# Optimization experiments

Measured on AMD Instinct MI355X. Metric: run time of the kernel, lower is better.

Reference implementation:

```python
import jax, jax.numpy as jnp
import numpy as np

B, S, E, H = 4, 2048, 1024, 16
D = E // H  # head dim = 64


def setup_inputs() -> dict:
    key = jax.random.key(0)
    ks = jax.random.split(key, 5)
    scale = 0.02
    return {
        "x": jax.random.normal(ks[0], (B, S, E), dtype=jnp.float32),
        "Wa_w": jax.random.normal(ks[1], (3 * E, E), dtype=jnp.float32) * scale,
        "Wa_b": jax.random.normal(ks[2], (3 * E,), dtype=jnp.float32) * scale,
        "Wo_w": jax.random.normal(ks[3], (E, E), dtype=jnp.float32) * scale,
        "Wo_b": jax.random.normal(ks[4], (E,), dtype=jnp.float32) * scale,
    }


def reference(x, Wa_w, Wa_b, Wo_w, Wo_b):
    b, s, e = x.shape
    # Fused QKV projection (torch Linear: x @ W^T + b)
    qkv = jnp.einsum("bse,fe->bsf", x, Wa_w) + Wa_b  # [B,S,3E]
    q, k, v = jnp.split(qkv, 3, axis=-1)
    # [B,S,E] -> [B,H,S,D]
    def heads(t):
        return t.reshape(b, s, H, D).transpose(0, 2, 1, 3)
    q, k, v = heads(q), heads(k), heads(v)
    # Causal attention with explicit score matrix (as in the original)
    scores = jnp.einsum("bhqd,bhkd->bhqk", q, k) / jnp.sqrt(jnp.float32(D))
    causal = jnp.tril(jnp.ones((s, s), dtype=bool))
    scores = jnp.where(causal, scores, -jnp.inf)
    attn = jax.nn.softmax(scores, axis=-1)  # dropout p=0 -> identity
    out = jnp.einsum("bhqk,bhkd->bhqd", attn, v)  # [B,H,S,D]
    out = out.transpose(0, 2, 1, 3).reshape(b, s, e)
    return jnp.einsum("bse,fe->bsf", out, Wo_w) + Wo_b
```

## Files before the change

### kernel.cpp

```cpp
#include <hip/hip_runtime.h>
#include <hip/hip_bf16.h>
#include <cstdint>

typedef __bf16 bf16_t;
typedef __attribute__((ext_vector_type(8))) __bf16 bf16x8;
typedef __attribute__((ext_vector_type(4))) __bf16 bf16x4;
typedef __attribute__((ext_vector_type(4))) float f32x4;

#define B_ 4
#define S_ 2048
#define E_ 1024
#define H_ 16
#define D_ 64

#define QSCALE 0.18033688011112042f

__global__ void cvt_f32_to_bf16(const float* __restrict__ in, bf16_t* __restrict__ out, int n4) {
    int i = blockIdx.x * blockDim.x + threadIdx.x;
    int stride = gridDim.x * blockDim.x;
    for (; i < n4; i += stride) {
        f32x4 v = reinterpret_cast<const f32x4*>(in)[i];
        bf16x4 o;
        o.x = (bf16_t)v.x; o.y = (bf16_t)v.y; o.z = (bf16_t)v.z; o.w = (bf16_t)v.w;
        reinterpret_cast<bf16x4*>(out)[i] = o;
    }
}

__device__ __forceinline__ void gload_lds16(const bf16_t* g, bf16_t* l) {
    __builtin_amdgcn_global_load_lds((const __attribute__((address_space(1))) void*)g,
                                     (__attribute__((address_space(3))) void*)l, 16, 0, 0);
}

template <int MODE>
__launch_bounds__(256)
__global__ void gemm_bt(const bf16_t* __restrict__ A, const bf16_t* __restrict__ Bm,
                        const float* __restrict__ bias,
                        int M, int N, int K,
                        bf16_t* __restrict__ Qg, bf16_t* __restrict__ Kg,
                        bf16_t* __restrict__ Vtg, float* __restrict__ Outf) {
    const int BM = 128, BN = 128, BK = 32;
    __shared__ __align__(16) bf16_t As[2][BM * BK];
    __shared__ __align__(16) bf16_t Bs[2][BN * BK];

    const int nwg = gridDim.x;
    const int cpx = nwg >> 3;
    const int bid = (blockIdx.x & 7) * cpx + (blockIdx.x >> 3);

    const int nTilesN = N / BN;
    const int mt = bid / nTilesN, nt = bid % nTilesN;
    const int m0 = mt * BM, n0 = nt * BN;
    const int t = threadIdx.x;
    const int lane = t & 63;
    const int wid = t >> 6;
    const int wr = wid >> 1, wc = wid & 1;
    const int lr = lane & 15, lg = lane >> 4;

    const int row = t >> 2;
    const int chunk = t & 3;
    const bf16_t* aSrc0 = A + (int64_t)(m0 + row) * K + chunk * 8;
    const bf16_t* bSrc0 = Bm + (int64_t)(n0 + row) * K + chunk * 8;
    const int ldsOff = row * BK + chunk * 8;

    auto stage = [&](int buf, int kt) {
        const bf16_t* a = aSrc0 + kt * BK;
        const bf16_t* b = bSrc0 + kt * BK;
        gload_lds16(a, &As[buf][ldsOff]);
        gload_lds16(a + (int64_t)64 * K, &As[buf][ldsOff + 64 * BK]);
        gload_lds16(b, &Bs[buf][ldsOff]);
        gload_lds16(b + (int64_t)64 * K, &Bs[buf][ldsOff + 64 * BK]);
    };

    f32x4 acc[4][4] = {};

    stage(0, 0);
    __syncthreads();
    const int nk = K / BK;
    for (int kt = 0; kt < nk; ++kt) {
        int buf = kt & 1;
        if (kt + 1 < nk) stage(buf ^ 1, kt + 1);
        bf16x8 af[4], bfr[4];
        const int ko = lg * 8;
#pragma unroll
        for (int i = 0; i < 4; ++i) {
            af[i]  = *(const bf16x8*)&As[buf][(wr * 64 + i * 16 + lr) * BK + ko];
            bfr[i] = *(const bf16x8*)&Bs[buf][(wc * 64 + i * 16 + lr) * BK + ko];
        }
#pragma unroll
        for (int i = 0; i < 4; ++i)
#pragma unroll
            for (int j = 0; j < 4; ++j)
                acc[i][j] = __builtin_amdgcn_mfma_f32_16x16x32_bf16(af[i], bfr[j], acc[i][j], 0, 0, 0);
        __syncthreads();
    }

    if (MODE == 0) {
        const int which = n0 / E_;
#pragma unroll
        for (int j = 0; j < 4; ++j) {
            const int f = n0 + wc * 64 + j * 16 + lr;
            const float bv = bias[f];
            const int fe = f - which * E_;
            const int h = fe >> 6, d = fe & 63;
#pragma unroll
            for (int i = 0; i < 4; ++i) {
#pragma unroll
                for (int r = 0; r < 4; ++r) {
                    const int m = m0 + wr * 64 + i * 16 + lg * 4 + r;
                    const int b = m >> 11, si = m & (S_ - 1);
                    const float v = acc[i][j][r] + bv;
                    if (which == 0)
                        Qg[(((int64_t)(b * H_ + h)) * S_ + si) * D_ + d] = (bf16_t)(v * QSCALE);
                    else if (which == 1)
                        Kg[(((int64_t)(b * H_ + h)) * S_ + si) * D_ + d] = (bf16_t)v;
                    else
                        Vtg[(((int64_t)(b * H_ + h)) * D_ + d) * S_ + si] = (bf16_t)v;
                }
            }
        }
    } else {
#pragma unroll
        for (int j = 0; j < 4; ++j) {
            const int f = n0 + wc * 64 + j * 16 + lr;
            const float bv = bias[f];
#pragma unroll
            for (int i = 0; i < 4; ++i) {
#pragma unroll
                for (int r = 0; r < 4; ++r) {
                    const int m = m0 + wr * 64 + i * 16 + lg * 4 + r;
                    Outf[(int64_t)m * N + f] = acc[i][j][r] + bv;
                }
            }
        }
    }
}

__launch_bounds__(256, 4)
__global__ void attn_causal(const bf16_t* __restrict__ Qg, const bf16_t* __restrict__ Kg,
                            const bf16_t* __restrict__ Vtg, bf16_t* __restrict__ Og) {
    __shared__ __align__(16) bf16_t Ks[2][64 * 64];
    __shared__ __align__(16) bf16_t Vs[2][64 * 64];
    __shared__ __align__(16) bf16_t P_lds[4][16 * 64];

    const int bid = blockIdx.x;
    const int xcd = bid & 7, j = bid >> 3;
    const int bh = (j >> 4) * 8 + xcd;
    const int i = j & 15;
    const int qtA = i, qtB = 31 - i;

    const int t = threadIdx.x, lane = t & 63, w = t >> 6;
    const int lr = lane & 15, lg = lane >> 4;
    const int q0A = qtA * 64 + w * 16;
    const int q0B = qtB * 64 + w * 16;

    const bf16_t* Qb = Qg + (int64_t)bh * S_ * D_;
    const bf16_t* Kb = Kg + (int64_t)bh * S_ * D_;
    const bf16_t* Vb = Vtg + (int64_t)bh * D_ * S_;

    const int srow = t >> 3;
    const int scol_sw = (t & 7) ^ (srow & 7);

    auto stageK = [&](int buf, int kv0) {
        const bf16_t* base = Kb + (kv0 + srow) * D_ + scol_sw * 8;
        gload_lds16(base, &Ks[buf][t * 8]);
        gload_lds16(base + 32 * D_, &Ks[buf][t * 8 + 2048]);
    };
    auto stageV = [&](int buf, int kv0) {
        const bf16_t* base = Vb + srow * S_ + kv0 + scol_sw * 8;
        gload_lds16(base, &Vs[buf][t * 8]);
        gload_lds16(base + 32 * S_, &Vs[buf][t * 8 + 2048]);
    };

    auto psw = [](int row, int col) {
        return row * 64 + ((((col >> 3) ^ (row & 7)) << 3) | (col & 7));
    };

    bf16x8 qfA[2], qfB[2];
#pragma unroll
    for (int kk = 0; kk < 2; ++kk) {
        qfA[kk] = *(const bf16x8*)&Qb[(q0A + lr) * D_ + kk * 32 + lg * 8];
        qfB[kk] = *(const bf16x8*)&Qb[(q0B + lr) * D_ + kk * 32 + lg * 8];
    }

    bf16x8 ones;
#pragma unroll
    for (int e = 0; e < 8; ++e) ones[e] = (bf16_t)1.0f;

    f32x4 oA[4] = {}, oB[4] = {};
    f32x4 lA = {}, lB = {};

    int cur = 0;
    stageK(0, 0);
    stageV(0, 0);
    __syncthreads();

    for (int tkv = 0; tkv <= qtB; ++tkv) {
        const int kv0 = tkv * 64;
        if (tkv < qtB) { stageK(cur ^ 1, kv0 + 64); stageV(cur ^ 1, kv0 + 64); }

        auto process = [&](int q0, const bf16x8* qf, f32x4* o, f32x4& accl, bf16_t* Pw) {
            f32x4 sc[4] = {};
            __builtin_amdgcn_s_setprio(1);
#pragma unroll
            for (int nj = 0; nj < 4; ++nj) {
                if (kv0 + nj * 16 <= q0 + 15) {
                    const int krow = nj * 16 + lr;
#pragma unroll
                    for (int kk = 0; kk < 2; ++kk) {
                        bf16x8 kfr = *(const bf16x8*)&Ks[cur][krow * 64 + (((kk * 4 + lg) ^ (krow & 7)) * 8)];
                        sc[nj] = __builtin_amdgcn_mfma_f32_16x16x32_bf16(qf[kk], kfr, sc[nj], 0, 0, 0);
                    }
                }
            }
            __builtin_amdgcn_s_setprio(0);

            if (kv0 + 64 > q0) {
#pragma unroll
                for (int nj = 0; nj < 4; ++nj) {
                    const int col = kv0 + nj * 16 + lr;
#pragma unroll
                    for (int r = 0; r < 4; ++r) {
                        const int rowg = q0 + lg * 4 + r;
                        if (col > rowg) sc[nj][r] = -1e30f;
                    }
                }
            }

#pragma unroll
            for (int nj = 0; nj < 4; ++nj)
#pragma unroll
                for (int r = 0; r < 4; ++r)
                    Pw[psw(lg * 4 + r, nj * 16 + lr)] = (bf16_t)__builtin_amdgcn_exp2f(sc[nj][r]);
            asm volatile("s_waitcnt lgkmcnt(0)" ::: "memory");
            __builtin_amdgcn_sched_barrier(0);

            __builtin_amdgcn_s_setprio(1);
#pragma unroll
            for (int kk = 0; kk < 2; ++kk) {
                bf16x8 pa = *(const bf16x8*)&Pw[psw(lr, kk * 32 + lg * 8)];
                accl = __builtin_amdgcn_mfma_f32_16x16x32_bf16(pa, ones, accl, 0, 0, 0);
#pragma unroll
                for (int nd = 0; nd < 4; ++nd) {
                    const int vrow = nd * 16 + lr;
                    bf16x8 vf = *(const bf16x8*)&Vs[cur][vrow * 64 + (((kk * 4 + lg) ^ (vrow & 7)) * 8)];
                    o[nd] = __builtin_amdgcn_mfma_f32_16x16x32_bf16(pa, vf, o[nd], 0, 0, 0);
                }
            }
            __builtin_amdgcn_s_setprio(0);
        };

        process(q0B, qfB, oB, lB, &P_lds[w][0]);
        if (tkv <= qtA) process(q0A, qfA, oA, lA, &P_lds[w][0]);

        __syncthreads();
        cur ^= 1;
    }

    const int b = bh >> 4, h = bh & 15;
#pragma unroll
    for (int r = 0; r < 4; ++r) {
        const float rlA = 1.0f / lA[r];
        const float rlB = 1.0f / lB[r];
        const int rA = q0A + lg * 4 + r;
        const int rB = q0B + lg * 4 + r;
#pragma unroll
        for (int nd = 0; nd < 4; ++nd) {
            Og[((int64_t)(b * S_ + rA)) * E_ + h * D_ + nd * 16 + lr] = (bf16_t)(oA[nd][r] * rlA);
            Og[((int64_t)(b * S_ + rB)) * E_ + h * D_ + nd * 16 + lr] = (bf16_t)(oB[nd][r] * rlB);
        }
    }
}

extern "C" void kernel_launch(void* const* d_in, const int* in_sizes, int n_in,
                              void* d_out, int out_size, void* d_ws, size_t ws_size,
                              hipStream_t stream) {
    const float* x    = (const float*)d_in[0];
    const float* Wa_w = (const float*)d_in[1];
    const float* Wa_b = (const float*)d_in[2];
    const float* Wo_w = (const float*)d_in[3];
    const float* Wo_b = (const float*)d_in[4];
    float* out = (float*)d_out;

    const size_t M = (size_t)B_ * S_;
    char* ws = (char*)d_ws;
    bf16_t* xb  = (bf16_t*)ws; ws += M * E_ * 2;
    bf16_t* wab = (bf16_t*)ws; ws += (size_t)3 * E_ * E_ * 2;
    bf16_t* wob = (bf16_t*)ws; ws += (size_t)E_ * E_ * 2;
    bf16_t* Qg  = (bf16_t*)ws; ws += M * E_ * 2;
    bf16_t* Kg  = (bf16_t*)ws; ws += M * E_ * 2;
    bf16_t* Vtg = (bf16_t*)ws; ws += M * E_ * 2;
    bf16_t* Og  = (bf16_t*)ws; ws += M * E_ * 2;

    cvt_f32_to_bf16<<<2048, 256, 0, stream>>>(x, xb, (int)(M * E_ / 4));
    cvt_f32_to_bf16<<<768, 256, 0, stream>>>(Wa_w, wab, 3 * E_ * E_ / 4);
    cvt_f32_to_bf16<<<256, 256, 0, stream>>>(Wo_w, wob, E_ * E_ / 4);

    gemm_bt<0><<<(8192 / 128) * (3072 / 128), 256, 0, stream>>>(
        xb, wab, Wa_b, 8192, 3072, 1024, Qg, Kg, Vtg, nullptr);

    attn_causal<<<B_ * H_ * 16, 256, 0, stream>>>(Qg, Kg, Vtg, Og);

    gemm_bt<1><<<(8192 / 128) * (1024 / 128), 256, 0, stream>>>(
        Og, wob, Wo_b, 8192, 1024, 1024, nullptr, nullptr, nullptr, out);
}
```

Measured before the change: 197.4 us.

## Rewrite projection GEMMs with 3-stage LDS pipeline, swizzled layout, larger tiles

Replaces the double-buffered 128x128 GEMM with a 512-thread 128x256 tile kernel that uses a three-buffer global-to-LDS pipeline. It waits with explicit vmcnt counts and a single barrier per k-step instead of a full sync, and stores LDS data in an XOR-swizzled layout to reduce bank conflicts on fragment reads. MFMA sections run at raised wave priority. The aim is better overlap of loads with MFMA and more reuse per tile, at the cost of more LDS per block and fewer blocks for the output GEMM.

```diff
diff --git a/kernel.cpp b/kernel.cpp
--- a/kernel.cpp
+++ b/kernel.cpp
@@ -31,70 +31,94 @@
                                      (__attribute__((address_space(3))) void*)l, 16, 0, 0);
 }
 
+__device__ __forceinline__ void wait_vm3() { asm volatile("s_waitcnt vmcnt(3)" ::: "memory"); }
+__device__ __forceinline__ void wait_vm0() { asm volatile("s_waitcnt vmcnt(0)" ::: "memory"); }
+
 template <int MODE>
-__launch_bounds__(256)
-__global__ void gemm_bt(const bf16_t* __restrict__ A, const bf16_t* __restrict__ Bm,
-                        const float* __restrict__ bias,
-                        int M, int N, int K,
-                        bf16_t* __restrict__ Qg, bf16_t* __restrict__ Kg,
-                        bf16_t* __restrict__ Vtg, float* __restrict__ Outf) {
-    const int BM = 128, BN = 128, BK = 32;
-    __shared__ __align__(16) bf16_t As[2][BM * BK];
-    __shared__ __align__(16) bf16_t Bs[2][BN * BK];
+__launch_bounds__(512, 2)
+__global__ void gemm_pipe(const bf16_t* __restrict__ A, const bf16_t* __restrict__ Bm,
+                          const float* __restrict__ bias,
+                          int M, int N,
+                          bf16_t* __restrict__ Qg, bf16_t* __restrict__ Kg,
+                          bf16_t* __restrict__ Vtg, float* __restrict__ Outf) {
+    constexpr int K = 1024, BK = 32, NKT = K / BK;
+    constexpr int BM = 128, BN = 256;
+    __shared__ __align__(16) bf16_t As[3][BM * BK];
+    __shared__ __align__(16) bf16_t Bs[3][BN * BK];
 
     const int nwg = gridDim.x;
     const int cpx = nwg >> 3;
     const int bid = (blockIdx.x & 7) * cpx + (blockIdx.x >> 3);
 
-    const int nTilesN = N / BN;
-    const int mt = bid / nTilesN, nt = bid % nTilesN;
+    const int nTN = N / BN;
+    const int mt = bid / nTN, nt = bid % nTN;
     const int m0 = mt * BM, n0 = nt * BN;
+
     const int t = threadIdx.x;
     const int lane = t & 63;
     const int wid = t >> 6;
-    const int wr = wid >> 1, wc = wid & 1;
+    const int wr = wid >> 2, wc = wid & 3;
     const int lr = lane & 15, lg = lane >> 4;
 
-    const int row = t >> 2;
-    const int chunk = t & 3;
-    const bf16_t* aSrc0 = A + (int64_t)(m0 + row) * K + chunk * 8;
-    const bf16_t* bSrc0 = Bm + (int64_t)(n0 + row) * K + chunk * 8;
-    const int ldsOff = row * BK + chunk * 8;
-
-    auto stage = [&](int buf, int kt) {
-        const bf16_t* a = aSrc0 + kt * BK;
-        const bf16_t* b = bSrc0 + kt * BK;
-        gload_lds16(a, &As[buf][ldsOff]);
-        gload_lds16(a + (int64_t)64 * K, &As[buf][ldsOff + 64 * BK]);
-        gload_lds16(b, &Bs[buf][ldsOff]);
-        gload_lds16(b + (int64_t)64 * K, &Bs[buf][ldsOff + 64 * BK]);
+    const int cA = t;
+    {
+    }
+    const int lineA = cA >> 3, chgA = (cA & 7) ^ (lineA & 7);
+    const bf16_t* aSrc = A + (int64_t)(m0 + 2 * lineA + (chgA >> 2)) * K + (chgA & 3) * 8;
+
+    const int cB0 = t, cB1 = t + 512;
+    const int lineB0 = cB0 >> 3, chgB0 = (cB0 & 7) ^ (lineB0 & 7);
+    const int lineB1 = cB1 >> 3, chgB1 = (cB1 & 7) ^ (lineB1 & 7);
+    const bf16_t* bSrc0 = Bm + (int64_t)(n0 + 2 * lineB0 + (chgB0 >> 2)) * K + (chgB0 & 3) * 8;
+    const bf16_t* bSrc1 = Bm + (int64_t)(n0 + 2 * lineB1 + (chgB1 >> 2)) * K + (chgB1 & 3) * 8;
+
+    auto stageT = [&](int kt, int buf) {
+        gload_lds16(aSrc + kt * BK, &As[buf][cA * 8]);
+        gload_lds16(bSrc0 + kt * BK, &Bs[buf][cB0 * 8]);
+        gload_lds16(bSrc1 + kt * BK, &Bs[buf][cB1 * 8]);
+    };
+
+    auto fragOff = [](int row, int kc) -> int {
+        const int line = row >> 1;
+        const int ch = ((row & 1) << 2) | kc;
+        return line * 64 + ((ch ^ (line & 7)) << 3);
     };
 
     f32x4 acc[4][4] = {};
 
-    stage(0, 0);
-    __syncthreads();
-    const int nk = K / BK;
-    for (int kt = 0; kt < nk; ++kt) {
-        int buf = kt & 1;
-        if (kt + 1 < nk) stage(buf ^ 1, kt + 1);
-        bf16x8 af[4], bfr[4];
-        const int ko = lg * 8;
-#pragma unroll
-        for (int i = 0; i < 4; ++i) {
-            af[i]  = *(const bf16x8*)&As[buf][(wr * 64 + i * 16 + lr) * BK + ko];
-            bfr[i] = *(const bf16x8*)&Bs[buf][(wc * 64 + i * 16 + lr) * BK + ko];
-        }
+    stageT(0, 0);
+    stageT(1, 1);
+
+    int bufc = 0, bufs = 2;
+    for (int kt = 0; kt < NKT; ++kt) {
+        if (kt < NKT - 1) wait_vm3(); else wait_vm0();
+        __builtin_amdgcn_s_barrier();
+        __builtin_amdgcn_sched_barrier(0);
+
+        if (kt + 2 < NKT) stageT(kt + 2, bufs);
+
+        bf16x8 bfr[4], afr[4];
+#pragma unroll
+        for (int j = 0; j < 4; ++j)
+            bfr[j] = *(const bf16x8*)&Bs[bufc][fragOff(wc * 64 + j * 16 + lr, lg)];
 #pragma unroll
         for (int i = 0; i < 4; ++i)
+            afr[i] = *(const bf16x8*)&As[bufc][fragOff(wr * 64 + i * 16 + lr, lg)];
+
+        __builtin_amdgcn_s_setprio(1);
+#pragma unroll
+        for (int i = 0; i < 4; ++i)
 #pragma unroll
             for (int j = 0; j < 4; ++j)
-                acc[i][j] = __builtin_amdgcn_mfma_f32_16x16x32_bf16(af[i], bfr[j], acc[i][j], 0, 0, 0);
-        __syncthreads();
+                acc[i][j] = __builtin_amdgcn_mfma_f32_16x16x32_bf16(afr[i], bfr[j], acc[i][j], 0, 0, 0);
+        __builtin_amdgcn_s_setprio(0);
+
+        bufc = (bufc == 2) ? 0 : bufc + 1;
+        bufs = (bufs == 2) ? 0 : bufs + 1;
     }
 
     if (MODE == 0) {
-        const int which = n0 / E_;
+        const int which = n0 >> 10;
 #pragma unroll
         for (int j = 0; j < 4; ++j) {
             const int f = n0 + wc * 64 + j * 16 + lr;
@@ -294,11 +318,11 @@
     cvt_f32_to_bf16<<<768, 256, 0, stream>>>(Wa_w, wab, 3 * E_ * E_ / 4);
     cvt_f32_to_bf16<<<256, 256, 0, stream>>>(Wo_w, wob, E_ * E_ / 4);
 
-    gemm_bt<0><<<(8192 / 128) * (3072 / 128), 256, 0, stream>>>(
-        xb, wab, Wa_b, 8192, 3072, 1024, Qg, Kg, Vtg, nullptr);
+    gemm_pipe<0><<<768, 512, 0, stream>>>(
+        xb, wab, Wa_b, 8192, 3072, Qg, Kg, Vtg, nullptr);
 
     attn_causal<<<B_ * H_ * 16, 256, 0, stream>>>(Qg, Kg, Vtg, Og);
 
-    gemm_bt<1><<<(8192 / 128) * (1024 / 128), 256, 0, stream>>>(
-        Og, wob, Wo_b, 8192, 1024, 1024, nullptr, nullptr, nullptr, out);
-}
+    gemm_pipe<1><<<256, 512, 0, stream>>>(
+        Og, wob, Wo_b, 8192, 1024, nullptr, nullptr, nullptr, out);
+}
```

New measurement: 229.1 us. 1.16x slower.
